# Optimization experiments

Hardware: AMD Instinct MI355X
Metric: run time of the kernel (lower is better)

## Reference

```python
import jax, jax.numpy as jnp
import numpy as np
from jax import lax

V, E, H, T = 100000, 256, 256, 8192
FL, FN, NC = 5, 128, 20


def setup_inputs() -> dict:
    key = jax.random.key(0)
    ks = jax.random.split(key, 12)
    s = 0.05
    return {
        "docs": jax.random.randint(ks[0], (1, T), 0, V),
        "docs_length": jnp.array([T]),
        "labels": jax.random.randint(ks[1], (1,), 0, NC),
        "iteration": 0,
        "embed_W": jax.random.uniform(ks[2], (V, E), jnp.float32, -0.1, 0.1),
        "w_ih": jax.random.normal(ks[3], (4 * H, E), jnp.float32) * s,
        "w_hh": jax.random.normal(ks[4], (4 * H, H), jnp.float32) * s,
        "b_ih": jax.random.normal(ks[5], (4 * H,), jnp.float32) * s,
        "b_hh": jax.random.normal(ks[6], (4 * H,), jnp.float32) * s,
        "conv_w": jax.random.normal(ks[7], (FN, 1, FL, H), jnp.float32) * s,
        "conv_b": jax.random.normal(ks[8], (FN,), jnp.float32) * s,
        "logits_w": jax.random.uniform(ks[9], (NC, FN), jnp.float32, -0.1, 0.1),
        "logits_b": jnp.zeros((NC,), jnp.float32),
    }


def _forward(docs, labels, embed_W, w_ih, w_hh, b_ih, b_hh, conv_w, conv_b, logits_w, logits_b):
    # embed -> ReLU (dropout is identity at p=0)
    x = jax.nn.relu(embed_W[docs[0]])  # (T, E)

    b = b_ih + b_hh

    def step(carry, xt):
        h, c = carry
        g = xt @ w_ih.T + h @ w_hh.T + b  # (4H,)
        i, f, gg, o = jnp.split(g, 4)
        i = jax.nn.sigmoid(i)
        f = jax.nn.sigmoid(f)
        gg = jnp.tanh(gg)
        o = jax.nn.sigmoid(o)
        c = f * c + i * gg
        h = o * jnp.tanh(c)
        return (h, c), h

    init = (jnp.zeros((H,), x.dtype), jnp.zeros((H,), x.dtype))
    _, hs = lax.scan(step, init, x)  # (T, H)

    # Conv2d(1, FN, (FL, H)) valid: (1,1,T,H) -> (1,FN,T-FL+1,1)
    feat = lax.conv_general_dilated(
        hs[None, None, :, :], conv_w, window_strides=(1, 1), padding="VALID",
        dimension_numbers=("NCHW", "OIHW", "NCHW"))
    feat = feat[0, :, :, 0] + conv_b[:, None]  # (FN, T-FL+1)

    # AdaptiveMaxPool2d((FN,1)) == max over time
    pooled = jnp.max(feat, axis=1)  # (FN,)

    logits = pooled @ logits_w.T + logits_b  # (NC,)
    logp = jax.nn.log_softmax(logits)
    loss = -logp[labels[0]]
    acc = (jnp.argmax(logp) == labels[0]).astype(jnp.float32)
    return loss, acc


def reference(docs, docs_length, labels, iteration, embed_W, w_ih, w_hh, b_ih, b_hh,
              conv_w, conv_b, logits_w, logits_b):
    return _forward(docs, labels, embed_W, w_ih, w_hh, b_ih, b_hh,
                    conv_w, conv_b, logits_w, logits_b)
```

## Files before the change

kernel.cpp:

```cpp
#include <hip/hip_runtime.h>
#include <math.h>

#define T_LEN 8192

typedef float f32x4 __attribute__((ext_vector_type(4)));
typedef int   i32x8 __attribute__((ext_vector_type(8)));
typedef int   i32x6 __attribute__((ext_vector_type(6)));

#define DPP_MAX(x, ctrl) fmaxf((x), __int_as_float(__builtin_amdgcn_update_dpp(0, __float_as_int(x), (ctrl), 0xF, 0xF, true)))

#define BAR_LDS() do { \
    __builtin_amdgcn_sched_barrier(0); \
    asm volatile("s_waitcnt lgkmcnt(0)" ::: "memory"); \
    __builtin_amdgcn_s_barrier(); \
    __builtin_amdgcn_sched_barrier(0); \
} while (0)

__device__ __forceinline__ float fexp2(float x) {
#if __has_builtin(__builtin_amdgcn_exp2f)
    return __builtin_amdgcn_exp2f(x);
#else
    return exp2f(x);
#endif
}
__device__ __forceinline__ float rcp1p(float e) {
    return __builtin_amdgcn_rcpf(1.f + e);
}
__device__ __forceinline__ float fsig_c(float x) {
    x = fminf(30.f, fmaxf(-30.f, x));
    float e = __expf(-x);
    return __builtin_amdgcn_rcpf(1.f + e);
}
__device__ __forceinline__ float ftanh_c(float x) {
    x = fminf(15.f, fmaxf(-15.f, x));
    float e = __expf(-2.f * x);
    return (1.f - e) * __builtin_amdgcn_rcpf(1.f + e);
}

__device__ __forceinline__ unsigned char enc_e4m3(float x) {
#if __has_builtin(__builtin_amdgcn_cvt_pk_fp8_f32)
    int v = __builtin_amdgcn_cvt_pk_fp8_f32(x, 0.f, 0, false);
    return (unsigned char)(v & 0xff);
#else
    unsigned u = __float_as_uint(x);
    unsigned s = (u >> 24) & 0x80u;
    float a = fabsf(x);
    if (a > 448.f) a = 448.f;
    if (a < 9.765625e-4f) return (unsigned char)s;
    int e = ((int)((__float_as_uint(a) >> 23) & 0xffu)) - 127;
    int eu = e < -6 ? -6 : e;
    float ulp = exp2f((float)(eu - 3));
    float q = rintf(a / ulp);
    int mant, ee;
    if (eu == -6 && q < 8.f) { mant = (int)q; ee = 0; }
    else {
        if (q >= 16.f) { q *= 0.5f; eu += 1; }
        mant = (int)q - 8; ee = eu + 7;
        if (ee > 15 || (ee == 15 && mant > 6)) { ee = 15; mant = 6; }
    }
    return (unsigned char)(s | (unsigned)(ee << 3) | (unsigned)mant);
#endif
}
__device__ __forceinline__ unsigned pk4(float a, float b, float c, float d) {
    return (unsigned)enc_e4m3(a) | ((unsigned)enc_e4m3(b) << 8)
         | ((unsigned)enc_e4m3(c) << 16) | ((unsigned)enc_e4m3(d) << 24);
}

__device__ __forceinline__ unsigned enc_e2m3(float x) {
    unsigned s = (__float_as_uint(x) >> 31) << 5;
    float a = fabsf(x);
    a = fminf(a, 7.5f);
    if (a < 0.0625f) return s;
    int e = ((int)((__float_as_uint(a) >> 23) & 0xffu)) - 127;
    int eu = e < 0 ? 0 : e;
    float ulp = __int_as_float((unsigned)(eu + 124) << 23);
    float q = rintf(a * __builtin_amdgcn_rcpf(ulp));
    int E, M;
    if (e < 0) {
        if (q >= 8.f) { E = 1; M = 0; }
        else { E = 0; M = (int)q; }
    } else {
        if (q >= 16.f) { q = 8.f; eu += 1; }
        if (eu > 2) { E = 3; M = 7; }
        else { E = eu + 1; M = (int)q - 8; }
    }
    return s | (unsigned)(E << 3) | (unsigned)M;
}

__device__ __forceinline__ int enc_e2m3_h4(float h) {
    float x = h * 4.f;
    float a = fabsf(x);
    int c1 = (int)rintf(a * 8.f);
    int c2 = (int)rintf(a * 4.f) + 8;
    int mag = (a < 2.f) ? c1 : c2;
    return mag | (int)((__float_as_uint(h) >> 26) & 32u);
}

__global__ __launch_bounds__(256) void pack_w6(
    const float* __restrict__ w_hh,
    unsigned* __restrict__ w6)
{
    int idx = blockIdx.x * 256 + threadIdx.x;
    int l  = idx & 63;
    int kt = (idx >> 6) & 1;
    int gt = idx >> 7;
    int rw = l & 15, kg = l >> 4;
    int rowp = (gt << 4) + rw;
    int orow = ((rowp & 3) << 8) + (rowp >> 2);
    const float* s = w_hh + (size_t)orow * 256 + 128 * kt + 32 * kg;
    unsigned d[6] = {0, 0, 0, 0, 0, 0};
#pragma unroll
    for (int j = 0; j < 32; ++j) {
        unsigned c = enc_e2m3(s[j] * 32.f);
        int bit = 6 * j;
        d[bit >> 5] |= c << (bit & 31);
        if ((bit & 31) > 26) d[(bit >> 5) + 1] |= c >> (32 - (bit & 31));
    }
    unsigned* o = w6 + (size_t)idx * 8;
    o[0] = d[0]; o[1] = d[1]; o[2] = d[2];
    o[3] = d[3]; o[4] = d[4]; o[5] = d[5];
    o[6] = 0;    o[7] = 0;
}

__global__ __launch_bounds__(256, 4) void gemm_pre(
    const int* __restrict__ docs,
    const float* __restrict__ embW,
    const float* __restrict__ w_ih,
    const float* __restrict__ b_ih,
    const float* __restrict__ b_hh,
    float* __restrict__ pre)
{
    __shared__ __align__(16) float As[16][68];
    __shared__ __align__(16) float Bs[16][68];
    __shared__ int rowid[64];
    const int bt = blockIdx.x;
    const int bj = blockIdx.y;
    const int tid = threadIdx.x;
    if (tid < 64) rowid[tid] = docs[bt * 64 + tid];
    __syncthreads();
    const int ti = tid & 15, tj = tid >> 4;
    const int r = tid & 63;
    const int kk4 = (tid >> 6) * 4;
    float acc[4][4];
#pragma unroll
    for (int ii = 0; ii < 4; ++ii)
#pragma unroll
        for (int jj = 0; jj < 4; ++jj) acc[ii][jj] = 0.f;

    for (int k0 = 0; k0 < 256; k0 += 16) {
        float4 av = *(const float4*)(embW + (size_t)rowid[r] * 256 + k0 + kk4);
        float4 bv = *(const float4*)(w_ih + (size_t)(bj * 64 + r) * 256 + k0 + kk4);
        As[kk4 + 0][r] = fmaxf(av.x, 0.f);
        As[kk4 + 1][r] = fmaxf(av.y, 0.f);
        As[kk4 + 2][r] = fmaxf(av.z, 0.f);
        As[kk4 + 3][r] = fmaxf(av.w, 0.f);
        Bs[kk4 + 0][r] = bv.x;
        Bs[kk4 + 1][r] = bv.y;
        Bs[kk4 + 2][r] = bv.z;
        Bs[kk4 + 3][r] = bv.w;
        __syncthreads();
#pragma unroll
        for (int kk = 0; kk < 16; ++kk) {
            float4 a = *(const float4*)&As[kk][ti * 4];
            float4 b = *(const float4*)&Bs[kk][tj * 4];
            acc[0][0] += a.x * b.x; acc[0][1] += a.x * b.y; acc[0][2] += a.x * b.z; acc[0][3] += a.x * b.w;
            acc[1][0] += a.y * b.x; acc[1][1] += a.y * b.y; acc[1][2] += a.y * b.z; acc[1][3] += a.y * b.w;
            acc[2][0] += a.z * b.x; acc[2][1] += a.z * b.y; acc[2][2] += a.z * b.z; acc[2][3] += a.z * b.w;
            acc[3][0] += a.w * b.x; acc[3][1] += a.w * b.y; acc[3][2] += a.w * b.z; acc[3][3] += a.w * b.w;
        }
        __syncthreads();
    }
#pragma unroll
    for (int ii = 0; ii < 4; ++ii) {
        int t = bt * 64 + ti * 4 + ii;
#pragma unroll
        for (int jj = 0; jj < 4; ++jj) {
            int j = bj * 64 + tj * 4 + jj;
            int jp = ((j & 255) << 2) | (j >> 8);
            pre[(size_t)t * 1024 + jp] = acc[ii][jj] + b_ih[j] + b_hh[j];
        }
    }
}

#define MFMA_PAIR(RT, DST) \
    asm("v_mfma_scale_f32_16x16x128_f8f6f4 %0, %1, %2, %5, %6, %6 cbsz:2 blgp:2\n\t" \
        "v_mfma_scale_f32_16x16x128_f8f6f4 %0, %3, %4, %0, %6, %6 cbsz:2 blgp:2" \
        : "=&v"(DST) \
        : "a"(wA[RT][0]), "v"(bq0), "a"(wA[RT][1]), "v"(bq1), "v"(CZ), "v"(sc))

__global__ __launch_bounds__(256, 1) void lstm_scan_mx6a(
    const float* __restrict__ pre,
    const unsigned* __restrict__ w6,
    float* __restrict__ hs)
{
    const int tid = threadIdx.x;
    const int w  = tid >> 6;
    const int l  = tid & 63;
    const int rto = l & 15;
    const int kg  = l >> 4;
    const float C_L2E  = -1.4426950408889634f;
    const float C_L2E2 = -2.8853900817779268f;
    const float I_L2E  = C_L2E  / 128.f;
    const float I_L2E2 = C_L2E2 / 128.f;

    __shared__ __align__(32) unsigned char h6pk[2][256];

    i32x6 wA[16][2];
#pragma unroll
    for (int rtt = 0; rtt < 16; ++rtt) {
#pragma unroll
        for (int kt = 0; kt < 2; ++kt) {
            int gt = 16 * w + rtt;
            const unsigned* s = w6 + (size_t)((gt * 2 + kt) * 64 + l) * 8;
            uint4 lo = *(const uint4*)s;
            uint2 hi = *(const uint2*)(s + 4);
            i32x6 v;
            v[0] = (int)lo.x; v[1] = (int)lo.y; v[2] = (int)lo.z;
            v[3] = (int)lo.w; v[4] = (int)hi.x; v[5] = (int)hi.y;
            wA[rtt][kt] = v;
        }
    }

    for (int i = tid; i < 512; i += 256) ((unsigned char*)h6pk)[i] = 0;

    const int u = 64 * w + 4 * rto + kg;
    float c_st = 0.f;

    const bool b0 = (rto & 1), b1 = (rto & 2), b2 = (rto & 4), b3 = (rto & 8);

    const bool iswr = (l < 48);
    const int s_  = (l >= 24) ? 1 : 0;
    const int b_  = l - 24 * s_;
    const int j0  = (4 * b_) / 3;
    const int rsh = 8 * b_ - 6 * j0;
    const int j1  = j0 + 1;
    const int lj0 = 16 * (j0 & 3) + 8 * s_ + (j0 >> 2);
    const int lj1 = 16 * (j1 & 3) + 8 * s_ + (j1 >> 2);
    const int wofs = (2 * w + s_) * 32 + b_;

    f32x4 CZ = (f32x4){0.f, 0.f, 0.f, 0.f};
    asm("" : "+v"(CZ));
    int sc = 0x7f7f7f7f;

    f32x4 p4c = *(const f32x4*)(pre + 4 * u);
    float tx = p4c.x * C_L2E;
    float ty = p4c.y * C_L2E;
    float tz = p4c.z * C_L2E2;
    float tw = p4c.w * C_L2E;
    const float* pp = pre + 1024 + 4 * u;
    float* hsp = hs + u;
    const unsigned char* h6base = (const unsigned char*)h6pk;
    BAR_LDS();

#define LSTM_STEP(RD, WR) do { \
    f32x4 p4n = *(const f32x4*)pp; pp += 1024; \
    i32x6 bq0, bq1; \
    { \
        const unsigned char* bp0 = h6base + (RD) + kg * 32; \
        uint4 lo = *(const uint4*)bp0; \
        uint2 hi = *(const uint2*)(bp0 + 16); \
        bq0[0] = (int)lo.x; bq0[1] = (int)lo.y; bq0[2] = (int)lo.z; \
        bq0[3] = (int)lo.w; bq0[4] = (int)hi.x; bq0[5] = (int)hi.y; \
        const unsigned char* bp1 = bp0 + 128; \
        uint4 lo1 = *(const uint4*)bp1; \
        uint2 hi1 = *(const uint2*)(bp1 + 16); \
        bq1[0] = (int)lo1.x; bq1[1] = (int)lo1.y; bq1[2] = (int)lo1.z; \
        bq1[3] = (int)lo1.w; bq1[4] = (int)hi1.x; bq1[5] = (int)hi1.y; \
    } \
    f32x4 a0, a1, a2, a3, a4, a5, a6, a7, a8, a9, a10, a11, a12, a13, a14, a15; \
    MFMA_PAIR(0, a0);  MFMA_PAIR(1, a1);  MFMA_PAIR(2, a2);  MFMA_PAIR(3, a3); \
    MFMA_PAIR(4, a4);  MFMA_PAIR(5, a5);  MFMA_PAIR(6, a6);  MFMA_PAIR(7, a7); \
    MFMA_PAIR(8, a8);  MFMA_PAIR(9, a9);  MFMA_PAIR(10, a10); MFMA_PAIR(11, a11); \
    MFMA_PAIR(12, a12); MFMA_PAIR(13, a13); MFMA_PAIR(14, a14); MFMA_PAIR(15, a15); \
    asm volatile("s_nop 7\n\ts_nop 7\n\ts_nop 7" \
        : "+v"(a0), "+v"(a1), "+v"(a2), "+v"(a3), "+v"(a4), "+v"(a5), "+v"(a6), "+v"(a7), \
          "+v"(a8), "+v"(a9), "+v"(a10), "+v"(a11), "+v"(a12), "+v"(a13), "+v"(a14), "+v"(a15)); \
    f32x4 s0 = b0 ? a1  : a0; \
    f32x4 s1 = b0 ? a3  : a2; \
    f32x4 s2 = b0 ? a5  : a4; \
    f32x4 s3 = b0 ? a7  : a6; \
    f32x4 s4 = b0 ? a9  : a8; \
    f32x4 s5 = b0 ? a11 : a10; \
    f32x4 s6 = b0 ? a13 : a12; \
    f32x4 s7 = b0 ? a15 : a14; \
    f32x4 q0 = b1 ? s1 : s0; \
    f32x4 q1 = b1 ? s3 : s2; \
    f32x4 q2 = b1 ? s5 : s4; \
    f32x4 q3 = b1 ? s7 : s6; \
    f32x4 r0 = b2 ? q1 : q0; \
    f32x4 r1 = b2 ? q3 : q2; \
    f32x4 av = b3 ? r1 : r0; \
    float nx = p4n.x * C_L2E, ny = p4n.y * C_L2E; \
    float nz = p4n.z * C_L2E2, nw = p4n.w * C_L2E; \
    float si = rcp1p(fexp2(fmaf(av.x, I_L2E,  tx))); \
    float sf = rcp1p(fexp2(fmaf(av.y, I_L2E,  ty))); \
    float tg = 2.f * rcp1p(fexp2(fmaf(av.z, I_L2E2, tz))) - 1.f; \
    float so = rcp1p(fexp2(fmaf(av.w, I_L2E,  tw))); \
    c_st = sf * c_st + si * tg; \
    float h = so * (2.f * rcp1p(fexp2(c_st * C_L2E2)) - 1.f); \
    hsp[0] = h; hsp += 256; \
    int code = enc_e2m3_h4(h); \
    int c0 = __shfl(code, lj0, 64); \
    int c1 = __shfl(code, lj1, 64); \
    if (iswr) { \
        unsigned byte = (((unsigned)c0 >> rsh) | ((unsigned)c1 << (6 - rsh))) & 0xffu; \
        *((unsigned char*)h6pk + (WR) + wofs) = (unsigned char)byte; \
    } \
    tx = nx; ty = ny; tz = nz; tw = nw; \
    BAR_LDS(); \
} while (0)

    for (int t2 = 0; t2 < T_LEN; t2 += 2) {
        LSTM_STEP(256, 0);
        LSTM_STEP(0, 256);
    }
#undef LSTM_STEP
}

__global__ __launch_bounds__(512, 2) void lstm_scan_mx6(
    const float* __restrict__ pre,
    const unsigned* __restrict__ w6,
    float* __restrict__ hs)
{
    const int tid = threadIdx.x;
    const int w  = tid >> 6;
    const int l  = tid & 63;
    const int rw = l & 15;
    const int kg = l >> 4;
    const float INV = 1.f / 128.f;

    __shared__ __align__(16) unsigned char h6pk[2][256];
    __shared__ __align__(16) float ldsPre[2][1024];

    i32x8 wA[8][2];
#pragma unroll
    for (int rt = 0; rt < 8; ++rt) {
#pragma unroll
        for (int kt = 0; kt < 2; ++kt) {
            const unsigned* s = w6 + (size_t)(((w * 8 + rt) * 2 + kt) * 64 + l) * 8;
            uint4 lo = *(const uint4*)s;
            uint2 hi = *(const uint2*)(s + 4);
            i32x8 v;
            v[0] = (int)lo.x; v[1] = (int)lo.y; v[2] = (int)lo.z;
            v[3] = (int)lo.w; v[4] = (int)hi.x; v[5] = (int)hi.y;
            v[6] = 0; v[7] = 0;
            wA[rt][kt] = v;
        }
    }

    for (int i = tid; i < 512; i += 512) h6pk[0][i] = 0;
    {
        float2 p = *(const float2*)(pre + 2 * tid);
        *(float2*)&ldsPre[0][2 * tid] = p;
    }

    const bool isup = (rw < 8);
    const int u = 32 * w + 4 * (rw & 7) + kg;
    float c_st = 0.f;

    const bool iswr = (rw < 8) && (kg < 3);
    const int bby = 8 * kg + rw;
    const int j0  = (4 * bby) / 3;
    const int rsh = 8 * bby - 6 * j0;
    const int lj0 = 16 * (j0 & 3) + (j0 >> 2);
    const int j1  = j0 + 1;
    const int lj1 = 16 * (j1 & 3) + (j1 >> 2);

    const float* pnext = pre + 1024 + 2 * tid;
    float* hsp = hs + u;
    __syncthreads();

    for (int t = 0; t < T_LEN; ++t) {
        const int PW = t & 1;
        const int PR = PW ^ 1;

        f32x4 p4 = *(const f32x4*)&ldsPre[PW][4 * u];

        float2 pv = *(const float2*)pnext;
        if (t + 2 < T_LEN) pnext += 1024;

        i32x8 bq[2];
#pragma unroll
        for (int kt = 0; kt < 2; ++kt) {
            const unsigned char* bp = &h6pk[PR][(4 * kt + kg) * 32];
            uint4 lo = *(const uint4*)bp;
            uint2 hi = *(const uint2*)(bp + 16);
            i32x8 b;
            b[0] = (int)lo.x; b[1] = (int)lo.y; b[2] = (int)lo.z; b[3] = (int)lo.w;
            b[4] = (int)hi.x; b[5] = (int)hi.y; b[6] = 0; b[7] = 0;
            bq[kt] = b;
        }

        f32x4 acc[8];
#pragma unroll
        for (int rt = 0; rt < 8; ++rt) acc[rt] = (f32x4){0.f, 0.f, 0.f, 0.f};
#pragma unroll
        for (int rt = 0; rt < 8; ++rt)
#pragma unroll
            for (int kt = 0; kt < 2; ++kt)
                acc[rt] = __builtin_amdgcn_mfma_scale_f32_16x16x128_f8f6f4(
                    wA[rt][kt], bq[kt], acc[rt],
                    2, 2, 0, 0x7f7f7f7f, 0, 0x7f7f7f7f);

        int code = 0;
        if (isup) {
            f32x4 av = acc[0];
            av = (rw == 1) ? acc[1] : av;
            av = (rw == 2) ? acc[2] : av;
            av = (rw == 3) ? acc[3] : av;
            av = (rw == 4) ? acc[4] : av;
            av = (rw == 5) ? acc[5] : av;
            av = (rw == 6) ? acc[6] : av;
            av = (rw == 7) ? acc[7] : av;
            float gi = fmaf(av.x, INV, p4.x);
            float gf = fmaf(av.y, INV, p4.y);
            float gg = fmaf(av.z, INV, p4.z);
            float go = fmaf(av.w, INV, p4.w);
            float si = fsig_c(gi);
            float sf = fsig_c(gf);
            float tg = ftanh_c(gg);
            float so = fsig_c(go);
            c_st = sf * c_st + si * tg;
            float h = so * ftanh_c(c_st);
            hsp[0] = h;
            code = (int)enc_e2m3(h * 4.f);
        }
        hsp += 256;

        int c0 = __shfl(code, lj0, 64);
        int c1 = __shfl(code, lj1, 64);
        if (iswr) {
            unsigned byte = (((unsigned)c0 >> rsh) | ((unsigned)c1 << (6 - rsh))) & 0xffu;
            h6pk[PW][w * 32 + bby] = (unsigned char)byte;
        }

        *(float2*)&ldsPre[PR][2 * tid] = pv;

        __syncthreads();
    }
}

__global__ __launch_bounds__(512, 2) void lstm_scan_mx8(
    const float* __restrict__ pre,
    const float* __restrict__ w_hh,
    float* __restrict__ hs)
{
    const int tid = threadIdx.x;
    const int w  = tid >> 6;
    const int l  = tid & 63;
    const int rw = l & 15;
    const int kg = l >> 4;
    const float INV = 1.f / 32768.f;

    __shared__ __align__(16) unsigned char h8[2 * 256];
    __shared__ __align__(16) float ldsPre[2][1024];

    i32x8 wA[8][2];
#pragma unroll
    for (int rt = 0; rt < 8; ++rt) {
#pragma unroll
        for (int kt = 0; kt < 2; ++kt) {
            int rowp = ((8 * w + rt) << 4) + rw;
            int orow = ((rowp & 3) << 8) + (rowp >> 2);
            const float* s = w_hh + (size_t)orow * 256 + 128 * kt + 32 * kg;
            i32x8 v;
#pragma unroll
            for (int d = 0; d < 8; ++d) {
                float4 f = *(const float4*)(s + 4 * d);
                v[d] = (int)pk4(f.x * 512.f, f.y * 512.f, f.z * 512.f, f.w * 512.f);
            }
            wA[rt][kt] = v;
        }
    }

    for (int i = tid; i < 512; i += 512) h8[i] = 0;
    {
        float2 p = *(const float2*)(pre + 2 * tid);
        *(float2*)&ldsPre[0][2 * tid] = p;
    }
    float c_st = 0.f;
    const bool isup = (rw < 8);
    const int u = 32 * w + 4 * (rw & 7) + kg;
    const float* pnext = pre + 1024 + 2 * tid;
    float* hsp = hs + u;
    __syncthreads();

    for (int t = 0; t < T_LEN; ++t) {
        const int PW = t & 1;
        const int PR = PW ^ 1;

        f32x4 p4 = *(const f32x4*)&ldsPre[PW][4 * u];

        float2 pv = *(const float2*)pnext;
        if (t + 2 < T_LEN) pnext += 1024;

        i32x8 bq[2];
#pragma unroll
        for (int kt = 0; kt < 2; ++kt) {
            const unsigned char* bp = &h8[PR * 256 + 128 * kt + 32 * kg];
            uint4 lo = *(const uint4*)bp;
            uint4 hi = *(const uint4*)(bp + 16);
            i32x8 b;
            b[0] = (int)lo.x; b[1] = (int)lo.y; b[2] = (int)lo.z; b[3] = (int)lo.w;
            b[4] = (int)hi.x; b[5] = (int)hi.y; b[6] = (int)hi.z; b[7] = (int)hi.w;
            bq[kt] = b;
        }

        f32x4 acc[8];
#pragma unroll
        for (int rt = 0; rt < 8; ++rt) acc[rt] = (f32x4){0.f, 0.f, 0.f, 0.f};
#pragma unroll
        for (int rt = 0; rt < 8; ++rt)
#pragma unroll
            for (int kt = 0; kt < 2; ++kt)
                acc[rt] = __builtin_amdgcn_mfma_scale_f32_16x16x128_f8f6f4(
                    wA[rt][kt], bq[kt], acc[rt],
                    0, 0, 0, 0x7f7f7f7f, 0, 0x7f7f7f7f);

        if (isup) {
            f32x4 av = acc[0];
            av = (rw == 1) ? acc[1] : av;
            av = (rw == 2) ? acc[2] : av;
            av = (rw == 3) ? acc[3] : av;
            av = (rw == 4) ? acc[4] : av;
            av = (rw == 5) ? acc[5] : av;
            av = (rw == 6) ? acc[6] : av;
            av = (rw == 7) ? acc[7] : av;
            float gi = fmaf(av.x, INV, p4.x);
            float gf = fmaf(av.y, INV, p4.y);
            float gg = fmaf(av.z, INV, p4.z);
            float go = fmaf(av.w, INV, p4.w);
            float si = fsig_c(gi);
            float sf = fsig_c(gf);
            float tg = ftanh_c(gg);
            float so = fsig_c(go);
            c_st = sf * c_st + si * tg;
            float h = so * ftanh_c(c_st);
            hsp[0] = h;
            h8[PW * 256 + u] = enc_e4m3(h * 64.f);
        }
        hsp += 256;

        *(float2*)&ldsPre[PR][2 * tid] = pv;

        __syncthreads();
    }
}

__global__ __launch_bounds__(256) void conv_pool(
    const float* __restrict__ hs,
    const float* __restrict__ cw,
    const float* __restrict__ cb,
    float* __restrict__ part)
{
    __shared__ __align__(16) float hst[68 * 260];
    __shared__ __align__(16) float cwS[128 * 68];
    const int blk = blockIdx.x;
    const int t0 = blk * 64;
    const int tid = threadIdx.x;
    const int i = tid & 15;
    const int g = tid >> 4;

    for (int e = tid; e < 68 * 64; e += 256) {
        int rr = e >> 6;
        int c4 = (e & 63) * 4;
        int tg = t0 + rr; if (tg > 8191) tg = 8191;
        float4 v = *(const float4*)(hs + (size_t)tg * 256 + c4);
        *(float4*)&hst[rr * 260 + c4] = v;
    }

    float acc[4][8];
#pragma unroll
    for (int tt = 0; tt < 4; ++tt)
#pragma unroll
        for (int j = 0; j < 8; ++j) acc[tt][j] = 0.f;

    for (int l = 0; l < 5; ++l) {
        for (int hc = 0; hc < 4; ++hc) {
            __syncthreads();
            {
                int n = tid >> 1;
                int hb = (tid & 1) * 32;
                const float* src = cw + (size_t)n * 1280 + l * 256 + hc * 64 + hb;
                float* dst = &cwS[n * 68 + hb];
#pragma unroll
                for (int q = 0; q < 8; ++q) {
                    float4 v = *(const float4*)(src + 4 * q);
                    *(float4*)(dst + 4 * q) = v;
                }
            }
            __syncthreads();
#pragma unroll 4
            for (int q = 0; q < 16; ++q) {
                float4 hvv[4];
#pragma unroll
                for (int tt = 0; tt < 4; ++tt)
                    hvv[tt] = *(const float4*)&hst[(i + 16 * tt + l) * 260 + hc * 64 + 4 * q];
#pragma unroll
                for (int j = 0; j < 8; ++j) {
                    float4 wv = *(const float4*)&cwS[(g + 16 * j) * 68 + 4 * q];
#pragma unroll
                    for (int tt = 0; tt < 4; ++tt) {
                        acc[tt][j] += hvv[tt].x * wv.x + hvv[tt].y * wv.y
                                    + hvv[tt].z * wv.z + hvv[tt].w * wv.w;
                    }
                }
            }
        }
    }

    float m[8];
#pragma unroll
    for (int j = 0; j < 8; ++j) {
        int n = g + 16 * j;
        float cbn = cb[n];
        float mm = -INFINITY;
#pragma unroll
        for (int tt = 0; tt < 4; ++tt) {
            int t = t0 + i + 16 * tt;
            float v = acc[tt][j] + cbn;
            if (t < 8188) mm = fmaxf(mm, v);
        }
        mm = DPP_MAX(mm, 0xB1);
        mm = DPP_MAX(mm, 0x4E);
        mm = DPP_MAX(mm, 0x141);
        mm = DPP_MAX(mm, 0x140);
        m[j] = mm;
    }
    if (i == 0) {
#pragma unroll
        for (int j = 0; j < 8; ++j)
            part[(size_t)blk * 128 + g + 16 * j] = m[j];
    }
}

__global__ void final_head(
    const float* __restrict__ part,
    const float* __restrict__ logits_w,
    const float* __restrict__ logits_b,
    const int* __restrict__ labels,
    float* __restrict__ out)
{
    __shared__ float pooled[128];
    __shared__ float lgt[20];
    int tid = threadIdx.x;
    float mx = -INFINITY;
    for (int b = 0; b < 128; ++b) mx = fmaxf(mx, part[(size_t)b * 128 + tid]);
    pooled[tid] = mx;
    __syncthreads();
    if (tid < 20) {
        float s = logits_b[tid];
        for (int k = 0; k < 128; ++k) s += logits_w[tid * 128 + k] * pooled[k];
        lgt[tid] = s;
    }
    __syncthreads();
    if (tid == 0) {
        float m = lgt[0]; int am = 0;
        for (int c2 = 1; c2 < 20; ++c2) { if (lgt[c2] > m) { m = lgt[c2]; am = c2; } }
        float se = 0.f;
        for (int c2 = 0; c2 < 20; ++c2) se += expf(lgt[c2] - m);
        float lse = m + logf(se);
        int lbl = labels[0];
        out[0] = -(lgt[lbl] - lse);
        out[1] = (am == lbl) ? 1.f : 0.f;
    }
}

extern "C" void kernel_launch(void* const* d_in, const int* in_sizes, int n_in,
                              void* d_out, int out_size, void* d_ws, size_t ws_size,
                              hipStream_t stream) {
    (void)in_sizes; (void)n_in; (void)out_size;
    const int*   docs   = (const int*)d_in[0];
    const int*   labels = (const int*)d_in[2];
    const float* embW   = (const float*)d_in[4];
    const float* w_ih   = (const float*)d_in[5];
    const float* w_hh   = (const float*)d_in[6];
    const float* b_ih   = (const float*)d_in[7];
    const float* b_hh   = (const float*)d_in[8];
    const float* cw     = (const float*)d_in[9];
    const float* cb     = (const float*)d_in[10];
    const float* lw     = (const float*)d_in[11];
    const float* lb     = (const float*)d_in[12];
    float* out = (float*)d_out;

    char* ws = (char*)d_ws;
    float*    pre  = (float*)(ws);
    float*    hs   = (float*)(ws + 33554432);
    float*    part = (float*)(ws + 41943040);
    unsigned* w6   = (unsigned*)(ws + 42008576);

    bool ws_ok = (ws_size >= (size_t)42270720);
    hipFuncAttributes aA, a6;
    bool okA = ws_ok
        && (hipFuncGetAttributes(&aA, (const void*)lstm_scan_mx6a) == hipSuccess)
        && (aA.localSizeBytes == 0);
    bool ok6 = ws_ok
        && (hipFuncGetAttributes(&a6, (const void*)lstm_scan_mx6) == hipSuccess)
        && (a6.localSizeBytes == 0);

    gemm_pre<<<dim3(128, 16, 1), 256, 0, stream>>>(docs, embW, w_ih, b_ih, b_hh, pre);
    if (okA || ok6) {
        pack_w6<<<32, 256, 0, stream>>>(w_hh, w6);
        if (okA) lstm_scan_mx6a<<<1, 256, 0, stream>>>(pre, w6, hs);
        else     lstm_scan_mx6<<<1, 512, 0, stream>>>(pre, w6, hs);
    } else {
        lstm_scan_mx8<<<1, 512, 0, stream>>>(pre, w_hh, hs);
    }
    conv_pool<<<128, 256, 0, stream>>>(hs, cw, cb, part);
    final_head<<<1, 128, 0, stream>>>(part, lw, lb, labels, out);
}
```

Baseline: 5.519 ms.

## Add mx6b LSTM scan with new weight layout and DPP-based h packing

Adds a new single-block LSTM scan kernel and matching weight packer. The weight rows are permuted so each lane's gate outputs are picked by a binary select tree interleaved with the MFMA issue, instead of needing 16 accumulators live before selection. The h code exchange uses a DPP lane rotate in place of two cross-lane shuffles, which removes ds_bpermute latency from the serial per-step chain. The old 512-thread mx6 path is removed and mx6b becomes the preferred path. The risks are correctness of the new permutation and the hand-inserted nops for the MFMA result hazard.

```diff
diff --git a/kernel.cpp b/kernel.cpp
--- a/kernel.cpp
+++ b/kernel.cpp
@@ -8,6 +8,7 @@
 typedef int   i32x6 __attribute__((ext_vector_type(6)));
 
 #define DPP_MAX(x, ctrl) fmaxf((x), __int_as_float(__builtin_amdgcn_update_dpp(0, __float_as_int(x), (ctrl), 0xF, 0xF, true)))
+#define SB() __builtin_amdgcn_sched_barrier(0)
 
 #define BAR_LDS() do { \
     __builtin_amdgcn_sched_barrier(0); \
@@ -96,7 +97,7 @@
     return mag | (int)((__float_as_uint(h) >> 26) & 32u);
 }
 
-__global__ __launch_bounds__(256) void pack_w6(
+__global__ __launch_bounds__(256) void pack_w6b(
     const float* __restrict__ w_hh,
     unsigned* __restrict__ w6)
 {
@@ -104,10 +105,35 @@
     int l  = idx & 63;
     int kt = (idx >> 6) & 1;
     int gt = idx >> 7;
-    int rw = l & 15, kg = l >> 4;
+    int rw = l & 15, ks = l >> 4;
+    int orow = ((rw & 3) << 8) + 64 * (gt >> 4) + (gt & 15) + 16 * (rw >> 2);
+    const float* s = w_hh + (size_t)orow * 256 + 128 * kt + 32 * ks;
+    unsigned d[6] = {0, 0, 0, 0, 0, 0};
+#pragma unroll
+    for (int j = 0; j < 32; ++j) {
+        unsigned c = enc_e2m3(s[j] * 32.f);
+        int bit = 6 * j;
+        d[bit >> 5] |= c << (bit & 31);
+        if ((bit & 31) > 26) d[(bit >> 5) + 1] |= c >> (32 - (bit & 31));
+    }
+    unsigned* o = w6 + (size_t)idx * 8;
+    o[0] = d[0]; o[1] = d[1]; o[2] = d[2];
+    o[3] = d[3]; o[4] = d[4]; o[5] = d[5];
+    o[6] = 0;    o[7] = 0;
+}
+
+__global__ __launch_bounds__(256) void pack_w6a(
+    const float* __restrict__ w_hh,
+    unsigned* __restrict__ w6)
+{
+    int idx = blockIdx.x * 256 + threadIdx.x;
+    int l  = idx & 63;
+    int kt = (idx >> 6) & 1;
+    int gt = idx >> 7;
+    int rw = l & 15, ks = l >> 4;
     int rowp = (gt << 4) + rw;
     int orow = ((rowp & 3) << 8) + (rowp >> 2);
-    const float* s = w_hh + (size_t)orow * 256 + 128 * kt + 32 * kg;
+    const float* s = w_hh + (size_t)orow * 256 + 128 * kt + 32 * ks;
     unsigned d[6] = {0, 0, 0, 0, 0, 0};
 #pragma unroll
     for (int j = 0; j < 32; ++j) {
@@ -187,6 +213,133 @@
         "v_mfma_scale_f32_16x16x128_f8f6f4 %0, %3, %4, %0, %6, %6 cbsz:2 blgp:2" \
         : "=&v"(DST) \
         : "a"(wA[RT][0]), "v"(bq0), "a"(wA[RT][1]), "v"(bq1), "v"(CZ), "v"(sc))
+
+__global__ __launch_bounds__(256, 1) void lstm_scan_mx6b(
+    const float* __restrict__ pre,
+    const unsigned* __restrict__ w6,
+    float* __restrict__ hs)
+{
+    const int tid = threadIdx.x;
+    const int w  = tid >> 6;
+    const int l  = tid & 63;
+    const int rto = l & 15;
+    const int kgr = l >> 4;
+    const float C_L2E  = -1.4426950408889634f;
+    const float C_L2E2 = -2.8853900817779268f;
+    const float I_L2E  = C_L2E  / 128.f;
+    const float I_L2E2 = C_L2E2 / 128.f;
+
+    __shared__ __align__(32) unsigned char h6pk[2][256];
+
+    i32x6 wA[16][2];
+#pragma unroll
+    for (int rtt = 0; rtt < 16; ++rtt) {
+#pragma unroll
+        for (int kt = 0; kt < 2; ++kt) {
+            int gt = 16 * w + rtt;
+            const unsigned* s = w6 + (size_t)((gt * 2 + kt) * 64 + l) * 8;
+            uint4 lo = *(const uint4*)s;
+            uint2 hi = *(const uint2*)(s + 4);
+            i32x6 v;
+            v[0] = (int)lo.x; v[1] = (int)lo.y; v[2] = (int)lo.z;
+            v[3] = (int)lo.w; v[4] = (int)hi.x; v[5] = (int)hi.y;
+            wA[rtt][kt] = v;
+        }
+    }
+
+    for (int i = tid; i < 512; i += 256) ((unsigned char*)h6pk)[i] = 0;
+
+    const int u = 64 * w + rto + 16 * kgr;
+    float c_st = 0.f;
+
+    const bool b0 = (rto & 1), b1 = (rto & 2), b2 = (rto & 4), b3 = (rto & 8);
+
+    const int qi  = l & 3;
+    const bool iswr = (qi < 3);
+    const int rsh = 2 * qi;
+    const int qq  = l >> 2;
+    const int G   = 4 * (qq >> 2) + (qq & 3);
+    const int wofs = (2 * w + (G >> 3)) * 32 + 3 * (G & 7) + qi;
+
+    f32x4 CZ = (f32x4){0.f, 0.f, 0.f, 0.f};
+    asm("" : "+v"(CZ));
+    int sc = 0x7f7f7f7f;
+
+    f32x4 p4c = *(const f32x4*)(pre + 4 * u);
+    float tx = p4c.x * C_L2E;
+    float ty = p4c.y * C_L2E;
+    float tz = p4c.z * C_L2E2;
+    float tw = p4c.w * C_L2E;
+    const float* pp = pre + 1024 + 4 * u;
+    float* hsp = hs + u;
+    const unsigned char* h6base = (const unsigned char*)h6pk;
+    BAR_LDS();
+
+#define LSTM_STEP(RD, WR) do { \
+    f32x4 p4n = *(const f32x4*)pp; pp += 1024; \
+    i32x6 bq0, bq1; \
+    { \
+        const unsigned char* bp0 = h6base + (RD) + kgr * 32; \
+        uint4 lo = *(const uint4*)bp0; \
+        uint2 hi = *(const uint2*)(bp0 + 16); \
+        bq0[0] = (int)lo.x; bq0[1] = (int)lo.y; bq0[2] = (int)lo.z; \
+        bq0[3] = (int)lo.w; bq0[4] = (int)hi.x; bq0[5] = (int)hi.y; \
+        const unsigned char* bp1 = bp0 + 128; \
+        uint4 lo1 = *(const uint4*)bp1; \
+        uint2 hi1 = *(const uint2*)(bp1 + 16); \
+        bq1[0] = (int)lo1.x; bq1[1] = (int)lo1.y; bq1[2] = (int)lo1.z; \
+        bq1[3] = (int)lo1.w; bq1[4] = (int)hi1.x; bq1[5] = (int)hi1.y; \
+    } \
+    f32x4 a0, a1, a2, a3, a4, a5, a6, a7, a8, a9, a10, a11, a12, a13, a14, a15; \
+    MFMA_PAIR(0, a0);  MFMA_PAIR(1, a1);  MFMA_PAIR(2, a2);  MFMA_PAIR(3, a3); \
+    SB(); \
+    f32x4 s0 = b0 ? a1 : a0; \
+    MFMA_PAIR(4, a4);  MFMA_PAIR(5, a5);  SB(); \
+    f32x4 s1 = b0 ? a3 : a2; \
+    MFMA_PAIR(6, a6);  MFMA_PAIR(7, a7);  SB(); \
+    f32x4 s2 = b0 ? a5 : a4; \
+    MFMA_PAIR(8, a8);  MFMA_PAIR(9, a9);  SB(); \
+    f32x4 s3 = b0 ? a7 : a6; \
+    f32x4 q0 = b1 ? s1 : s0; \
+    MFMA_PAIR(10, a10); MFMA_PAIR(11, a11); SB(); \
+    f32x4 s4 = b0 ? a9 : a8; \
+    MFMA_PAIR(12, a12); MFMA_PAIR(13, a13); SB(); \
+    f32x4 s5 = b0 ? a11 : a10; \
+    f32x4 q1 = b1 ? s3 : s2; \
+    MFMA_PAIR(14, a14); MFMA_PAIR(15, a15); SB(); \
+    f32x4 s6 = b0 ? a13 : a12; \
+    asm volatile("s_nop 7\n\ts_nop 7" : "+v"(a14), "+v"(a15)); \
+    f32x4 s7 = b0 ? a15 : a14; \
+    f32x4 q2 = b1 ? s5 : s4; \
+    f32x4 q3 = b1 ? s7 : s6; \
+    f32x4 r0 = b2 ? q1 : q0; \
+    f32x4 r1 = b2 ? q3 : q2; \
+    f32x4 av = b3 ? r1 : r0; \
+    float nx = p4n.x * C_L2E, ny = p4n.y * C_L2E; \
+    float nz = p4n.z * C_L2E2, nw = p4n.w * C_L2E; \
+    float si = rcp1p(fexp2(fmaf(av.x, I_L2E,  tx))); \
+    float sf = rcp1p(fexp2(fmaf(av.y, I_L2E,  ty))); \
+    float tg = 2.f * rcp1p(fexp2(fmaf(av.z, I_L2E2, tz))) - 1.f; \
+    float so = rcp1p(fexp2(fmaf(av.w, I_L2E,  tw))); \
+    c_st = sf * c_st + si * tg; \
+    float h = so * (2.f * rcp1p(fexp2(c_st * C_L2E2)) - 1.f); \
+    hsp[0] = h; hsp += 256; \
+    int code = enc_e2m3_h4(h); \
+    int cnx = __builtin_amdgcn_update_dpp(0, code, 0x39, 0xF, 0xF, true); \
+    if (iswr) { \
+        unsigned byte = (((unsigned)code >> rsh) | ((unsigned)cnx << (6 - rsh))) & 0xffu; \
+        *((unsigned char*)h6pk + (WR) + wofs) = (unsigned char)byte; \
+    } \
+    tx = nx; ty = ny; tz = nz; tw = nw; \
+    BAR_LDS(); \
+} while (0)
+
+    for (int t2 = 0; t2 < T_LEN; t2 += 2) {
+        LSTM_STEP(256, 0);
+        LSTM_STEP(0, 256);
+    }
+#undef LSTM_STEP
+}
 
 __global__ __launch_bounds__(256, 1) void lstm_scan_mx6a(
     const float* __restrict__ pre,
@@ -317,129 +470,6 @@
 #undef LSTM_STEP
 }
 
-__global__ __launch_bounds__(512, 2) void lstm_scan_mx6(
-    const float* __restrict__ pre,
-    const unsigned* __restrict__ w6,
-    float* __restrict__ hs)
-{
-    const int tid = threadIdx.x;
-    const int w  = tid >> 6;
-    const int l  = tid & 63;
-    const int rw = l & 15;
-    const int kg = l >> 4;
-    const float INV = 1.f / 128.f;
-
-    __shared__ __align__(16) unsigned char h6pk[2][256];
-    __shared__ __align__(16) float ldsPre[2][1024];
-
-    i32x8 wA[8][2];
-#pragma unroll
-    for (int rt = 0; rt < 8; ++rt) {
-#pragma unroll
-        for (int kt = 0; kt < 2; ++kt) {
-            const unsigned* s = w6 + (size_t)(((w * 8 + rt) * 2 + kt) * 64 + l) * 8;
-            uint4 lo = *(const uint4*)s;
-            uint2 hi = *(const uint2*)(s + 4);
-            i32x8 v;
-            v[0] = (int)lo.x; v[1] = (int)lo.y; v[2] = (int)lo.z;
-            v[3] = (int)lo.w; v[4] = (int)hi.x; v[5] = (int)hi.y;
-            v[6] = 0; v[7] = 0;
-            wA[rt][kt] = v;
-        }
-    }
-
-    for (int i = tid; i < 512; i += 512) h6pk[0][i] = 0;
-    {
-        float2 p = *(const float2*)(pre + 2 * tid);
-        *(float2*)&ldsPre[0][2 * tid] = p;
-    }
-
-    const bool isup = (rw < 8);
-    const int u = 32 * w + 4 * (rw & 7) + kg;
-    float c_st = 0.f;
-
-    const bool iswr = (rw < 8) && (kg < 3);
-    const int bby = 8 * kg + rw;
-    const int j0  = (4 * bby) / 3;
-    const int rsh = 8 * bby - 6 * j0;
-    const int lj0 = 16 * (j0 & 3) + (j0 >> 2);
-    const int j1  = j0 + 1;
-    const int lj1 = 16 * (j1 & 3) + (j1 >> 2);
-
-    const float* pnext = pre + 1024 + 2 * tid;
-    float* hsp = hs + u;
-    __syncthreads();
-
-    for (int t = 0; t < T_LEN; ++t) {
-        const int PW = t & 1;
-        const int PR = PW ^ 1;
-
-        f32x4 p4 = *(const f32x4*)&ldsPre[PW][4 * u];
-
-        float2 pv = *(const float2*)pnext;
-        if (t + 2 < T_LEN) pnext += 1024;
-
-        i32x8 bq[2];
-#pragma unroll
-        for (int kt = 0; kt < 2; ++kt) {
-            const unsigned char* bp = &h6pk[PR][(4 * kt + kg) * 32];
-            uint4 lo = *(const uint4*)bp;
-            uint2 hi = *(const uint2*)(bp + 16);
-            i32x8 b;
-            b[0] = (int)lo.x; b[1] = (int)lo.y; b[2] = (int)lo.z; b[3] = (int)lo.w;
-            b[4] = (int)hi.x; b[5] = (int)hi.y; b[6] = 0; b[7] = 0;
-            bq[kt] = b;
-        }
-
-        f32x4 acc[8];
-#pragma unroll
-        for (int rt = 0; rt < 8; ++rt) acc[rt] = (f32x4){0.f, 0.f, 0.f, 0.f};
-#pragma unroll
-        for (int rt = 0; rt < 8; ++rt)
-#pragma unroll
-            for (int kt = 0; kt < 2; ++kt)
-                acc[rt] = __builtin_amdgcn_mfma_scale_f32_16x16x128_f8f6f4(
-                    wA[rt][kt], bq[kt], acc[rt],
-                    2, 2, 0, 0x7f7f7f7f, 0, 0x7f7f7f7f);
-
-        int code = 0;
-        if (isup) {
-            f32x4 av = acc[0];
-            av = (rw == 1) ? acc[1] : av;
-            av = (rw == 2) ? acc[2] : av;
-            av = (rw == 3) ? acc[3] : av;
-            av = (rw == 4) ? acc[4] : av;
-            av = (rw == 5) ? acc[5] : av;
-            av = (rw == 6) ? acc[6] : av;
-            av = (rw == 7) ? acc[7] : av;
-            float gi = fmaf(av.x, INV, p4.x);
-            float gf = fmaf(av.y, INV, p4.y);
-            float gg = fmaf(av.z, INV, p4.z);
-            float go = fmaf(av.w, INV, p4.w);
-            float si = fsig_c(gi);
-            float sf = fsig_c(gf);
-            float tg = ftanh_c(gg);
-            float so = fsig_c(go);
-            c_st = sf * c_st + si * tg;
-            float h = so * ftanh_c(c_st);
-            hsp[0] = h;
-            code = (int)enc_e2m3(h * 4.f);
-        }
-        hsp += 256;
-
-        int c0 = __shfl(code, lj0, 64);
-        int c1 = __shfl(code, lj1, 64);
-        if (iswr) {
-            unsigned byte = (((unsigned)c0 >> rsh) | ((unsigned)c1 << (6 - rsh))) & 0xffu;
-            h6pk[PW][w * 32 + bby] = (unsigned char)byte;
-        }
-
-        *(float2*)&ldsPre[PR][2 * tid] = pv;
-
-        __syncthreads();
-    }
-}
-
 __global__ __launch_bounds__(512, 2) void lstm_scan_mx8(
     const float* __restrict__ pre,
     const float* __restrict__ w_hh,
@@ -690,19 +720,21 @@
     unsigned* w6   = (unsigned*)(ws + 42008576);
 
     bool ws_ok = (ws_size >= (size_t)42270720);
-    hipFuncAttributes aA, a6;
+    hipFuncAttributes aB, aA;
+    bool okB = ws_ok
+        && (hipFuncGetAttributes(&aB, (const void*)lstm_scan_mx6b) == hipSuccess)
+        && (aB.localSizeBytes == 0);
     bool okA = ws_ok
         && (hipFuncGetAttributes(&aA, (const void*)lstm_scan_mx6a) == hipSuccess)
         && (aA.localSizeBytes == 0);
-    bool ok6 = ws_ok
-        && (hipFuncGetAttributes(&a6, (const void*)lstm_scan_mx6) == hipSuccess)
-        && (a6.localSizeBytes == 0);
 
     gemm_pre<<<dim3(128, 16, 1), 256, 0, stream>>>(docs, embW, w_ih, b_ih, b_hh, pre);
-    if (okA || ok6) {
-        pack_w6<<<32, 256, 0, stream>>>(w_hh, w6);
-        if (okA) lstm_scan_mx6a<<<1, 256, 0, stream>>>(pre, w6, hs);
-        else     lstm_scan_mx6<<<1, 512, 0, stream>>>(pre, w6, hs);
+    if (okB) {
+        pack_w6b<<<32, 256, 0, stream>>>(w_hh, w6);
+        lstm_scan_mx6b<<<1, 256, 0, stream>>>(pre, w6, hs);
+    } else if (okA) {
+        pack_w6a<<<32, 256, 0, stream>>>(w_hh, w6);
+        lstm_scan_mx6a<<<1, 256, 0, stream>>>(pre, w6, hs);
     } else {
         lstm_scan_mx8<<<1, 512, 0, stream>>>(pre, w_hh, hs);
     }
```

After: 5.125 ms. 1.08x faster.
